# Kernel optimization log

Measured on AMD Instinct MI355X. Metric: run time of the kernel, lower is better.

## Reference

```python
import jax, jax.numpy as jnp
import numpy as np

B, L, D_IN, D_H, D_OUT = 8, 1024, 1024, 1024, 1024


def setup_inputs() -> dict:
    key = jax.random.key(0)
    ks = jax.random.split(key, 9)
    s = 0.02  # weight scale to keep ReLU chain stable
    return {
        "leaves": jax.random.normal(ks[0], (B, L, D_IN), dtype=jnp.float32),
        "V_w": jax.random.normal(ks[1], (D_H, D_IN), dtype=jnp.float32) * s,
        "V_b": jax.random.normal(ks[2], (D_H,), dtype=jnp.float32) * s,
        "U_w": jax.random.normal(ks[3], (D_H, D_H), dtype=jnp.float32) * s,
        "U_b": jax.random.normal(ks[4], (D_H,), dtype=jnp.float32) * s,
        "W_w": jax.random.normal(ks[5], (D_H, D_H), dtype=jnp.float32) * s,
        "W_b": jax.random.normal(ks[6], (D_H,), dtype=jnp.float32) * s,
        "O_w": jax.random.normal(ks[7], (D_OUT, D_H), dtype=jnp.float32) * s,
        "O_b": jax.random.normal(ks[8], (D_OUT,), dtype=jnp.float32) * s,
    }


def reference(leaves, V_w, V_b, U_w, U_b, W_w, W_b, O_w, O_b):
    # Leaf encoding: h_leaf = relu(V(x))            [B, L, H]
    h = jax.nn.relu(jnp.einsum("bli,hi->blh", leaves, V_w) + V_b)
    # Depth-batched recursion over the complete binary tree:
    # combined = relu(U(left) + W(right)); log2(L) levels, node count halves.
    while h.shape[1] > 1:
        left, right = h[:, 0::2], h[:, 1::2]  # [B, n/2, H] each
        h = jax.nn.relu(
            jnp.einsum("bnh,gh->bng", left, U_w) + U_b
            + jnp.einsum("bnh,gh->bng", right, W_w) + W_b
        )
    root = h[:, 0]  # [B, H]
    logits = jnp.einsum("bh,oh->bo", root, O_w) + O_b
    return jax.nn.log_softmax(logits, axis=-1)
```

## Files before the change

kernel.cpp:

```cpp
#include <hip/hip_runtime.h>
#include <hip/hip_bf16.h>
#include <math.h>

typedef __bf16 bf16_t;
typedef __bf16 bf16x8 __attribute__((ext_vector_type(8)));
typedef __bf16 bf16x4 __attribute__((ext_vector_type(4)));
typedef float  f32x4  __attribute__((ext_vector_type(4)));

#define GLD_LDS16(g, l)                                                          \
  __builtin_amdgcn_global_load_lds((const __attribute__((address_space(1))) void*)(g), \
                                   (__attribute__((address_space(3))) void*)(l), 16, 0, 0)

__global__ __launch_bounds__(256) void k_cvt_all(const float* __restrict__ leaves,
                                                 const float* __restrict__ V_w,
                                                 const float* __restrict__ O_w,
                                                 const float* __restrict__ U_w,
                                                 const float* __restrict__ W_w,
                                                 const float* __restrict__ U_b,
                                                 const float* __restrict__ W_b,
                                                 bf16_t* __restrict__ leaves_bf,
                                                 bf16_t* __restrict__ Vw_bf,
                                                 bf16_t* __restrict__ Ow_bf,
                                                 bf16_t* __restrict__ UW_bf,
                                                 float* __restrict__ buw) {
  const int gtid = blockIdx.x * 256 + threadIdx.x;
  const int G = gridDim.x * 256;
  for (int i = gtid; i < 2097152; i += G) {
    float4 v = reinterpret_cast<const float4*>(leaves)[i];
    bf16x4 o; o[0] = (bf16_t)v.x; o[1] = (bf16_t)v.y; o[2] = (bf16_t)v.z; o[3] = (bf16_t)v.w;
    reinterpret_cast<bf16x4*>(leaves_bf)[i] = o;
  }
  for (int i = gtid; i < 262144; i += G) {
    float4 v = reinterpret_cast<const float4*>(V_w)[i];
    bf16x4 o; o[0] = (bf16_t)v.x; o[1] = (bf16_t)v.y; o[2] = (bf16_t)v.z; o[3] = (bf16_t)v.w;
    reinterpret_cast<bf16x4*>(Vw_bf)[i] = o;
  }
  for (int i = gtid; i < 262144; i += G) {
    float4 v = reinterpret_cast<const float4*>(O_w)[i];
    bf16x4 o; o[0] = (bf16_t)v.x; o[1] = (bf16_t)v.y; o[2] = (bf16_t)v.z; o[3] = (bf16_t)v.w;
    reinterpret_cast<bf16x4*>(Ow_bf)[i] = o;
  }
  for (int idx = gtid; idx < 524288; idx += G) {
    int i = idx * 4;
    int g = i >> 11;
    int k = i & 2047;
    const float* src = (k < 1024) ? (U_w + g * 1024 + k) : (W_w + g * 1024 + (k - 1024));
    float4 v = *reinterpret_cast<const float4*>(src);
    bf16x4 o; o[0] = (bf16_t)v.x; o[1] = (bf16_t)v.y; o[2] = (bf16_t)v.z; o[3] = (bf16_t)v.w;
    reinterpret_cast<bf16x4*>(UW_bf)[idx] = o;
  }
  if (gtid < 1024) buw[gtid] = U_b[gtid] + W_b[gtid];
}

template <bool SPLIT>
__global__ __launch_bounds__(512, 4) void k_gemm2(
    const bf16_t* __restrict__ A, const bf16_t* __restrict__ Bw,
    const float* __restrict__ bias, bf16_t* __restrict__ C,
    bf16_t* __restrict__ P, int M, int Kstride, int kchunk) {
  constexpr int NB = 5;
  constexpr int VM = 2;
  __shared__ bf16_t As[NB][128 * 32];
  __shared__ bf16_t Bs[NB][128 * 32];

  const int tid = threadIdx.x;
  const int lane = tid & 63;
  const int wave = tid >> 6;
  const int wr = wave >> 2;
  const int wc = wave & 3;
  const int bm = blockIdx.x, bn = blockIdx.y, bz = blockIdx.z;

  const bf16_t* Abase = A + (size_t)bm * 128 * Kstride + (size_t)bz * kchunk;
  const bf16_t* Bbase = Bw + (size_t)bn * 128 * Kstride + (size_t)bz * kchunk;

  f32x4 acc[4][2] = {};
  const int rl = lane & 15, kq = lane >> 4;

  auto stage = [&](int buf, int ko) {
    {
      int c = tid;
      int r = c >> 2, kbp = c & 3;
      int kb = kbp ^ ((r >> 1) & 3);
      GLD_LDS16(Abase + (size_t)r * Kstride + ko + kb * 8, &As[buf][c * 8]);
    }
    {
      int c = tid;
      int r = c >> 2, kbp = c & 3;
      int kb = kbp ^ ((r >> 1) & 3);
      GLD_LDS16(Bbase + (size_t)r * Kstride + ko + kb * 8, &Bs[buf][c * 8]);
    }
  };

  const int kiters = kchunk >> 5;
  stage(0, 0);
  if (kiters > 1) stage(1, 32);
  if (kiters > 2) stage(2, 64);
  if (kiters > 3) stage(3, 96);

  int cur = 0;
  for (int t = 0; t < kiters; ++t) {
    const int nin = kiters - 1 - t;
    if (nin >= 3)      asm volatile("s_waitcnt vmcnt(%0)" :: "i"(3 * VM) : "memory");
    else if (nin == 2) asm volatile("s_waitcnt vmcnt(%0)" :: "i"(2 * VM) : "memory");
    else if (nin == 1) asm volatile("s_waitcnt vmcnt(%0)" :: "i"(VM) : "memory");
    else               asm volatile("s_waitcnt vmcnt(0)" ::: "memory");
    __builtin_amdgcn_s_barrier();
    __builtin_amdgcn_sched_barrier(0);
    if (t + NB - 1 < kiters) {
      int bnx = cur + NB - 1; if (bnx >= NB) bnx -= NB;
      stage(bnx, (t + NB - 1) * 32);
    }
    bf16x8 af[4], bfr[2];
#pragma unroll
    for (int i = 0; i < 4; ++i) {
      int r = wr * 64 + i * 16 + rl;
      int kbp = kq ^ ((r >> 1) & 3);
      af[i] = *reinterpret_cast<const bf16x8*>(&As[cur][r * 32 + kbp * 8]);
    }
#pragma unroll
    for (int j = 0; j < 2; ++j) {
      int r = wc * 32 + j * 16 + rl;
      int kbp = kq ^ ((r >> 1) & 3);
      bfr[j] = *reinterpret_cast<const bf16x8*>(&Bs[cur][r * 32 + kbp * 8]);
    }
#pragma unroll
    for (int i = 0; i < 4; ++i)
#pragma unroll
      for (int j = 0; j < 2; ++j)
        acc[i][j] = __builtin_amdgcn_mfma_f32_16x16x32_bf16(af[i], bfr[j], acc[i][j], 0, 0, 0);
    if (++cur >= NB) cur = 0;
  }

  const int rq = lane >> 4, cl = lane & 15;
  if (SPLIT) {
    bf16_t* Pp = P + (size_t)bz * M * 1024;
#pragma unroll
    for (int j = 0; j < 2; ++j) {
      int gcol = bn * 128 + wc * 32 + j * 16 + cl;
#pragma unroll
      for (int i = 0; i < 4; ++i) {
        int grow = bm * 128 + wr * 64 + i * 16 + rq * 4;
#pragma unroll
        for (int reg = 0; reg < 4; ++reg)
          Pp[(size_t)(grow + reg) * 1024 + gcol] = (bf16_t)acc[i][j][reg];
      }
    }
  } else {
#pragma unroll
    for (int j = 0; j < 2; ++j) {
      int gcol = bn * 128 + wc * 32 + j * 16 + cl;
      float bv = bias[gcol];
#pragma unroll
      for (int i = 0; i < 4; ++i) {
        int grow = bm * 128 + wr * 64 + i * 16 + rq * 4;
#pragma unroll
        for (int reg = 0; reg < 4; ++reg) {
          float v = acc[i][j][reg] + bv;
          v = v > 0.0f ? v : 0.0f;
          C[(size_t)(grow + reg) * 1024 + gcol] = (bf16_t)v;
        }
      }
    }
  }
}

template <int TM, int TN, bool SPLIT>
__global__ __launch_bounds__(256, 3) void k_gemm(
    const bf16_t* __restrict__ A, const bf16_t* __restrict__ Bw,
    const float* __restrict__ bias, bf16_t* __restrict__ C,
    bf16_t* __restrict__ P, int M, int Kstride, int kchunk) {
  constexpr int MI = TM / 32;
  constexpr int NJ = TN / 32;
  constexpr int VM = TM / 64 + TN / 64;
  constexpr int NB = 4;
  __shared__ bf16_t As[NB][TM * 32];
  __shared__ bf16_t Bs[NB][TN * 32];

  const int tid = threadIdx.x;
  const int lane = tid & 63;
  const int wave = tid >> 6;
  const int wr = wave >> 1, wc = wave & 1;
  const int bm = blockIdx.x, bn = blockIdx.y, bz = blockIdx.z;

  const bf16_t* Abase = A + (size_t)bm * TM * Kstride + (size_t)bz * kchunk;
  const bf16_t* Bbase = Bw + (size_t)bn * TN * Kstride + (size_t)bz * kchunk;

  f32x4 acc[MI][NJ] = {};
  const int rl = lane & 15, kq = lane >> 4;

  auto stage = [&](int buf, int ko) {
#pragma unroll
    for (int it = 0; it < TM / 64; ++it) {
      int c = tid + 256 * it;
      int r = c >> 2, kbp = c & 3;
      int kb = kbp ^ ((r >> 1) & 3);
      GLD_LDS16(Abase + (size_t)r * Kstride + ko + kb * 8, &As[buf][c * 8]);
    }
#pragma unroll
    for (int it = 0; it < TN / 64; ++it) {
      int c = tid + 256 * it;
      int r = c >> 2, kbp = c & 3;
      int kb = kbp ^ ((r >> 1) & 3);
      GLD_LDS16(Bbase + (size_t)r * Kstride + ko + kb * 8, &Bs[buf][c * 8]);
    }
  };

  const int kiters = kchunk >> 5;
  stage(0, 0);
  if (kiters > 1) stage(1, 32);
  if (kiters > 2) stage(2, 64);

  int cur = 0;
  for (int t = 0; t < kiters; ++t) {
    const int nin = kiters - 1 - t;
    if (nin >= 2)      asm volatile("s_waitcnt vmcnt(%0)" :: "i"(2 * VM) : "memory");
    else if (nin == 1) asm volatile("s_waitcnt vmcnt(%0)" :: "i"(VM) : "memory");
    else               asm volatile("s_waitcnt vmcnt(0)" ::: "memory");
    __builtin_amdgcn_s_barrier();
    __builtin_amdgcn_sched_barrier(0);
    if (t + NB - 1 < kiters) {
      int bnx = cur + NB - 1; if (bnx >= NB) bnx -= NB;
      stage(bnx, (t + NB - 1) * 32);
    }
    bf16x8 af[MI], bfr[NJ];
#pragma unroll
    for (int i = 0; i < MI; ++i) {
      int r = wr * (TM / 2) + i * 16 + rl;
      int kbp = kq ^ ((r >> 1) & 3);
      af[i] = *reinterpret_cast<const bf16x8*>(&As[cur][r * 32 + kbp * 8]);
    }
#pragma unroll
    for (int j = 0; j < NJ; ++j) {
      int r = wc * (TN / 2) + j * 16 + rl;
      int kbp = kq ^ ((r >> 1) & 3);
      bfr[j] = *reinterpret_cast<const bf16x8*>(&Bs[cur][r * 32 + kbp * 8]);
    }
#pragma unroll
    for (int i = 0; i < MI; ++i)
#pragma unroll
      for (int j = 0; j < NJ; ++j)
        acc[i][j] = __builtin_amdgcn_mfma_f32_16x16x32_bf16(af[i], bfr[j], acc[i][j], 0, 0, 0);
    if (++cur >= NB) cur = 0;
  }

  const int rq = lane >> 4, cl = lane & 15;
  if (SPLIT) {
    bf16_t* Pp = P + (size_t)bz * M * 1024;
#pragma unroll
    for (int j = 0; j < NJ; ++j) {
      int gcol = bn * TN + wc * (TN / 2) + j * 16 + cl;
#pragma unroll
      for (int i = 0; i < MI; ++i) {
        int grow = bm * TM + wr * (TM / 2) + i * 16 + rq * 4;
#pragma unroll
        for (int reg = 0; reg < 4; ++reg)
          if (grow + reg < M)
            Pp[(size_t)(grow + reg) * 1024 + gcol] = (bf16_t)acc[i][j][reg];
      }
    }
  } else {
#pragma unroll
    for (int j = 0; j < NJ; ++j) {
      int gcol = bn * TN + wc * (TN / 2) + j * 16 + cl;
      float bv = bias[gcol];
#pragma unroll
      for (int i = 0; i < MI; ++i) {
        int grow = bm * TM + wr * (TM / 2) + i * 16 + rq * 4;
#pragma unroll
        for (int reg = 0; reg < 4; ++reg) {
          float v = acc[i][j][reg] + bv;
          v = v > 0.0f ? v : 0.0f;
          C[(size_t)(grow + reg) * 1024 + gcol] = (bf16_t)v;
        }
      }
    }
  }
}

__global__ __launch_bounds__(256) void k_reduce(const bf16_t* __restrict__ P,
                                                const float* __restrict__ bias,
                                                bf16_t* __restrict__ C, int M, int ks) {
  constexpr int N = 1024;
  int idx = blockIdx.x * 256 + threadIdx.x;
  int col = (idx * 4) & (N - 1);
  int row = (idx * 4) >> 10;
  float s0 = 0.0f, s1 = 0.0f, s2 = 0.0f, s3 = 0.0f;
  for (int z = 0; z < ks; ++z) {
    bf16x4 v = *reinterpret_cast<const bf16x4*>(P + ((size_t)z * M + row) * N + col);
    s0 += (float)v[0]; s1 += (float)v[1]; s2 += (float)v[2]; s3 += (float)v[3];
  }
  float4 b = *reinterpret_cast<const float4*>(bias + col);
  bf16x4 o;
  o[0] = (bf16_t)fmaxf(s0 + b.x, 0.0f);
  o[1] = (bf16_t)fmaxf(s1 + b.y, 0.0f);
  o[2] = (bf16_t)fmaxf(s2 + b.z, 0.0f);
  o[3] = (bf16_t)fmaxf(s3 + b.w, 0.0f);
  reinterpret_cast<bf16x4*>(C)[idx] = o;
}

template <int KK, bool RELU, bool F32OUT>
__global__ __launch_bounds__(256) void k_tail(const bf16_t* __restrict__ A,
                                              const bf16_t* __restrict__ Bw,
                                              const float* __restrict__ bias,
                                              void* __restrict__ Cout, int M) {
  constexpr int N = 1024;
  constexpr int KPL = KK / 64;
  const int lane = threadIdx.x & 63;
  const int gw = blockIdx.x * 4 + (threadIdx.x >> 6);
  const int n = gw & (N - 1);
  const int mbase = (gw >> 10) * 8;
  const int k0 = lane * KPL;

  float bv[KPL];
  const bf16_t* bp = Bw + (size_t)n * KK + k0;
#pragma unroll
  for (int q = 0; q < KPL / 8; ++q) {
    bf16x8 v = *reinterpret_cast<const bf16x8*>(bp + q * 8);
#pragma unroll
    for (int j = 0; j < 8; ++j) bv[q * 8 + j] = (float)v[j];
  }

  float acc[8];
#pragma unroll
  for (int m = 0; m < 8; ++m) {
    const bf16_t* ap = A + (size_t)(mbase + m) * KK + k0;
    float s = 0.0f;
#pragma unroll
    for (int q = 0; q < KPL / 8; ++q) {
      bf16x8 v = *reinterpret_cast<const bf16x8*>(ap + q * 8);
#pragma unroll
      for (int j = 0; j < 8; ++j) s += (float)v[j] * bv[q * 8 + j];
    }
    acc[m] = s;
  }
#pragma unroll
  for (int m = 0; m < 8; ++m) {
#pragma unroll
    for (int off = 32; off >= 1; off >>= 1) acc[m] += __shfl_xor(acc[m], off, 64);
  }
  if (lane < 8 && mbase + lane < M) {
    float v = acc[lane] + bias[n];
    if (RELU) v = v > 0.0f ? v : 0.0f;
    if (F32OUT) ((float*)Cout)[(size_t)(mbase + lane) * N + n] = v;
    else        ((bf16_t*)Cout)[(size_t)(mbase + lane) * N + n] = (bf16_t)v;
  }
}

__global__ __launch_bounds__(256) void k_logsoftmax(const float* __restrict__ logits,
                                                    float* __restrict__ out) {
  int b = blockIdx.x;
  const float* x = logits + b * 1024;
  int tid = threadIdx.x;
  int wave = tid >> 6, lane = tid & 63;
  __shared__ float red[8];

  float m = -1e30f;
  for (int i = tid; i < 1024; i += 256) m = fmaxf(m, x[i]);
#pragma unroll
  for (int off = 32; off >= 1; off >>= 1) m = fmaxf(m, __shfl_xor(m, off, 64));
  if (lane == 0) red[wave] = m;
  __syncthreads();
  m = fmaxf(fmaxf(red[0], red[1]), fmaxf(red[2], red[3]));
  float s = 0.0f;
  for (int i = tid; i < 1024; i += 256) s += expf(x[i] - m);
#pragma unroll
  for (int off = 32; off >= 1; off >>= 1) s += __shfl_xor(s, off, 64);
  if (lane == 0) red[wave] = s;
  __syncthreads();
  float lse = m + logf(red[0] + red[1] + red[2] + red[3]);
  for (int i = tid; i < 1024; i += 256) out[b * 1024 + i] = x[i] - lse;
}

extern "C" void kernel_launch(void* const* d_in, const int* in_sizes, int n_in,
                              void* d_out, int out_size, void* d_ws, size_t ws_size,
                              hipStream_t stream) {
  const float* leaves = (const float*)d_in[0];
  const float* V_w = (const float*)d_in[1];
  const float* V_b = (const float*)d_in[2];
  const float* U_w = (const float*)d_in[3];
  const float* U_b = (const float*)d_in[4];
  const float* W_w = (const float*)d_in[5];
  const float* W_b = (const float*)d_in[6];
  const float* O_w = (const float*)d_in[7];
  const float* O_b = (const float*)d_in[8];
  float* out = (float*)d_out;

  char* ws = (char*)d_ws;
  size_t off = 0;
  auto alloc = [&](size_t bytes) -> void* {
    off = (off + 255) & ~(size_t)255;
    void* p = ws + off;
    off += bytes;
    return p;
  };

  const size_t MB16 = (size_t)8192 * 1024 * 2;
  bf16_t* leaves_bf = (bf16_t*)alloc(MB16);
  bf16_t* Vw_bf = (bf16_t*)alloc((size_t)1024 * 1024 * 2);
  bf16_t* UW_bf = (bf16_t*)alloc((size_t)2 * 1024 * 1024 * 2);
  bf16_t* Ow_bf = (bf16_t*)alloc((size_t)1024 * 1024 * 2);
  float* buw = (float*)alloc(1024 * 4);
  bf16_t* hA = (bf16_t*)alloc(MB16);
  float* logits = (float*)alloc(8 * 1024 * 4);
  bf16_t* Pbuf = (bf16_t*)alloc((size_t)8 * 4096 * 1024 * 2);
  (void)ws_size; (void)in_sizes; (void)n_in; (void)out_size;

  k_cvt_all<<<2048, 256, 0, stream>>>(leaves, V_w, O_w, U_w, W_w, U_b, W_b,
                                      leaves_bf, Vw_bf, Ow_bf, UW_bf, buw);

  k_gemm2<false><<<dim3(64, 8), 512, 0, stream>>>(
      leaves_bf, Vw_bf, V_b, hA, nullptr, 8192, 1024, 1024);

  bf16_t* src = hA;
  bf16_t* dst = leaves_bf;
  auto swap = [&]() { bf16_t* t = src; src = dst; dst = t; };

  k_gemm2<true><<<dim3(32, 8, 2), 512, 0, stream>>>(
      src, UW_bf, nullptr, nullptr, Pbuf, 4096, 2048, 1024);
  k_reduce<<<4096 * 1024 / 4 / 256, 256, 0, stream>>>(Pbuf, buw, dst, 4096, 2);
  swap();
  k_gemm<64, 128, false><<<dim3(32, 8), 256, 0, stream>>>(
      src, UW_bf, buw, dst, nullptr, 2048, 2048, 2048);
  swap();
  k_gemm<64, 128, true><<<dim3(16, 8, 4), 256, 0, stream>>>(
      src, UW_bf, nullptr, nullptr, Pbuf, 1024, 2048, 512);
  k_reduce<<<1024 * 1024 / 4 / 256, 256, 0, stream>>>(Pbuf, buw, dst, 1024, 4);
  swap();
  k_gemm<64, 128, true><<<dim3(8, 8, 4), 256, 0, stream>>>(
      src, UW_bf, nullptr, nullptr, Pbuf, 512, 2048, 512);
  k_reduce<<<512 * 1024 / 4 / 256, 256, 0, stream>>>(Pbuf, buw, dst, 512, 4);
  swap();
  k_gemm<64, 128, true><<<dim3(4, 8, 8), 256, 0, stream>>>(
      src, UW_bf, nullptr, nullptr, Pbuf, 256, 2048, 256);
  k_reduce<<<256 * 1024 / 4 / 256, 256, 0, stream>>>(Pbuf, buw, dst, 256, 8);
  swap();
  k_gemm<64, 128, true><<<dim3(2, 8, 8), 256, 0, stream>>>(
      src, UW_bf, nullptr, nullptr, Pbuf, 128, 2048, 256);
  k_reduce<<<128 * 1024 / 4 / 256, 256, 0, stream>>>(Pbuf, buw, dst, 128, 8);
  swap();
  k_gemm<64, 128, true><<<dim3(1, 8, 16), 256, 0, stream>>>(
      src, UW_bf, nullptr, nullptr, Pbuf, 64, 2048, 128);
  k_reduce<<<64 * 1024 / 4 / 256, 256, 0, stream>>>(Pbuf, buw, dst, 64, 16);
  swap();
  k_gemm<64, 128, true><<<dim3(1, 8, 16), 256, 0, stream>>>(
      src, UW_bf, nullptr, nullptr, Pbuf, 32, 2048, 128);
  k_reduce<<<32 * 1024 / 4 / 256, 256, 0, stream>>>(Pbuf, buw, dst, 32, 16);
  swap();
  for (int M = 16; M >= 8; M >>= 1) {
    int blocks = (M / 8) * 1024 / 4;
    k_tail<2048, true, false><<<blocks, 256, 0, stream>>>(src, UW_bf, buw, dst, M);
    swap();
  }

  k_tail<1024, false, true><<<256, 256, 0, stream>>>(src, Ow_bf, O_b, logits, 8);
  k_logsoftmax<<<8, 256, 0, stream>>>(logits, out);
}
```

Baseline: 203.0 us.

## Rework GEMM wave tiling to 4 waves, add BK=64 small-tile kernel, split level two

The 128x128 GEMM now uses 4 waves, each computing a 64x64 sub-tile, instead of 8 waves each computing 64x32. That doubles per-wave register reuse of the A fragments. The 64x128 kernel now stages K=64 per stage with a wider XOR swizzle and 3 buffers, which halves the number of barrier iterations. The 2048-row level now uses a 2-way split-K plus a reduce pass instead of a single full-K kernel, to put more blocks in flight. Fewer waves per block lowers latency hiding, and the extra reduce pass adds memory traffic.

```diff
diff --git a/kernel.cpp b/kernel.cpp
--- a/kernel.cpp
+++ b/kernel.cpp
@@ -53,42 +53,45 @@
 }
 
 template <bool SPLIT>
-__global__ __launch_bounds__(512, 4) void k_gemm2(
+__global__ __launch_bounds__(256, 2) void k_gemm(
     const bf16_t* __restrict__ A, const bf16_t* __restrict__ Bw,
     const float* __restrict__ bias, bf16_t* __restrict__ C,
     bf16_t* __restrict__ P, int M, int Kstride, int kchunk) {
+  constexpr int VM = 3;
   constexpr int NB = 5;
-  constexpr int VM = 2;
   __shared__ bf16_t As[NB][128 * 32];
   __shared__ bf16_t Bs[NB][128 * 32];
 
   const int tid = threadIdx.x;
   const int lane = tid & 63;
   const int wave = tid >> 6;
-  const int wr = wave >> 2;
-  const int wc = wave & 3;
+  const int wr = wave >> 1, wc = wave & 1;
   const int bm = blockIdx.x, bn = blockIdx.y, bz = blockIdx.z;
 
   const bf16_t* Abase = A + (size_t)bm * 128 * Kstride + (size_t)bz * kchunk;
   const bf16_t* Bbase = Bw + (size_t)bn * 128 * Kstride + (size_t)bz * kchunk;
 
-  f32x4 acc[4][2] = {};
+  f32x4 acc[4][4] = {};
   const int rl = lane & 15, kq = lane >> 4;
+  constexpr int VMS = 4;
 
   auto stage = [&](int buf, int ko) {
-    {
-      int c = tid;
+#pragma unroll
+    for (int it = 0; it < 2; ++it) {
+      int c = tid + 256 * it;
       int r = c >> 2, kbp = c & 3;
       int kb = kbp ^ ((r >> 1) & 3);
       GLD_LDS16(Abase + (size_t)r * Kstride + ko + kb * 8, &As[buf][c * 8]);
     }
-    {
-      int c = tid;
+#pragma unroll
+    for (int it = 0; it < 2; ++it) {
+      int c = tid + 256 * it;
       int r = c >> 2, kbp = c & 3;
       int kb = kbp ^ ((r >> 1) & 3);
       GLD_LDS16(Bbase + (size_t)r * Kstride + ko + kb * 8, &Bs[buf][c * 8]);
     }
   };
+  (void)VM;
 
   const int kiters = kchunk >> 5;
   stage(0, 0);
@@ -99,9 +102,9 @@
   int cur = 0;
   for (int t = 0; t < kiters; ++t) {
     const int nin = kiters - 1 - t;
-    if (nin >= 3)      asm volatile("s_waitcnt vmcnt(%0)" :: "i"(3 * VM) : "memory");
-    else if (nin == 2) asm volatile("s_waitcnt vmcnt(%0)" :: "i"(2 * VM) : "memory");
-    else if (nin == 1) asm volatile("s_waitcnt vmcnt(%0)" :: "i"(VM) : "memory");
+    if (nin >= 3)      asm volatile("s_waitcnt vmcnt(%0)" :: "i"(3 * VMS) : "memory");
+    else if (nin == 2) asm volatile("s_waitcnt vmcnt(%0)" :: "i"(2 * VMS) : "memory");
+    else if (nin == 1) asm volatile("s_waitcnt vmcnt(%0)" :: "i"(VMS) : "memory");
     else               asm volatile("s_waitcnt vmcnt(0)" ::: "memory");
     __builtin_amdgcn_s_barrier();
     __builtin_amdgcn_sched_barrier(0);
@@ -109,7 +112,7 @@
       int bnx = cur + NB - 1; if (bnx >= NB) bnx -= NB;
       stage(bnx, (t + NB - 1) * 32);
     }
-    bf16x8 af[4], bfr[2];
+    bf16x8 af[4], bfr[4];
 #pragma unroll
     for (int i = 0; i < 4; ++i) {
       int r = wr * 64 + i * 16 + rl;
@@ -117,15 +120,15 @@
       af[i] = *reinterpret_cast<const bf16x8*>(&As[cur][r * 32 + kbp * 8]);
     }
 #pragma unroll
-    for (int j = 0; j < 2; ++j) {
-      int r = wc * 32 + j * 16 + rl;
+    for (int j = 0; j < 4; ++j) {
+      int r = wc * 64 + j * 16 + rl;
       int kbp = kq ^ ((r >> 1) & 3);
       bfr[j] = *reinterpret_cast<const bf16x8*>(&Bs[cur][r * 32 + kbp * 8]);
     }
 #pragma unroll
     for (int i = 0; i < 4; ++i)
 #pragma unroll
-      for (int j = 0; j < 2; ++j)
+      for (int j = 0; j < 4; ++j)
         acc[i][j] = __builtin_amdgcn_mfma_f32_16x16x32_bf16(af[i], bfr[j], acc[i][j], 0, 0, 0);
     if (++cur >= NB) cur = 0;
   }
@@ -134,8 +137,8 @@
   if (SPLIT) {
     bf16_t* Pp = P + (size_t)bz * M * 1024;
 #pragma unroll
-    for (int j = 0; j < 2; ++j) {
-      int gcol = bn * 128 + wc * 32 + j * 16 + cl;
+    for (int j = 0; j < 4; ++j) {
+      int gcol = bn * 128 + wc * 64 + j * 16 + cl;
 #pragma unroll
       for (int i = 0; i < 4; ++i) {
         int grow = bm * 128 + wr * 64 + i * 16 + rq * 4;
@@ -146,8 +149,8 @@
     }
   } else {
 #pragma unroll
-    for (int j = 0; j < 2; ++j) {
-      int gcol = bn * 128 + wc * 32 + j * 16 + cl;
+    for (int j = 0; j < 4; ++j) {
+      int gcol = bn * 128 + wc * 64 + j * 16 + cl;
       float bv = bias[gcol];
 #pragma unroll
       for (int i = 0; i < 4; ++i) {
@@ -163,17 +166,15 @@
   }
 }
 
-template <int TM, int TN, bool SPLIT>
-__global__ __launch_bounds__(256, 3) void k_gemm(
+template <bool SPLIT>
+__global__ __launch_bounds__(256, 2) void k_gemm64(
     const bf16_t* __restrict__ A, const bf16_t* __restrict__ Bw,
     const float* __restrict__ bias, bf16_t* __restrict__ C,
     bf16_t* __restrict__ P, int M, int Kstride, int kchunk) {
-  constexpr int MI = TM / 32;
-  constexpr int NJ = TN / 32;
-  constexpr int VM = TM / 64 + TN / 64;
-  constexpr int NB = 4;
-  __shared__ bf16_t As[NB][TM * 32];
-  __shared__ bf16_t Bs[NB][TN * 32];
+  constexpr int VM = 6;
+  constexpr int NB = 3;
+  __shared__ bf16_t As[NB][64 * 64];
+  __shared__ bf16_t Bs[NB][128 * 64];
 
   const int tid = threadIdx.x;
   const int lane = tid & 63;
@@ -181,76 +182,77 @@
   const int wr = wave >> 1, wc = wave & 1;
   const int bm = blockIdx.x, bn = blockIdx.y, bz = blockIdx.z;
 
-  const bf16_t* Abase = A + (size_t)bm * TM * Kstride + (size_t)bz * kchunk;
-  const bf16_t* Bbase = Bw + (size_t)bn * TN * Kstride + (size_t)bz * kchunk;
-
-  f32x4 acc[MI][NJ] = {};
+  const bf16_t* Abase = A + (size_t)bm * 64 * Kstride + (size_t)bz * kchunk;
+  const bf16_t* Bbase = Bw + (size_t)bn * 128 * Kstride + (size_t)bz * kchunk;
+
+  f32x4 acc[2][4] = {};
   const int rl = lane & 15, kq = lane >> 4;
 
   auto stage = [&](int buf, int ko) {
 #pragma unroll
-    for (int it = 0; it < TM / 64; ++it) {
+    for (int it = 0; it < 2; ++it) {
       int c = tid + 256 * it;
-      int r = c >> 2, kbp = c & 3;
-      int kb = kbp ^ ((r >> 1) & 3);
+      int r = c >> 3, ch = c & 7;
+      int kb = ch ^ ((r >> 1) & 7);
       GLD_LDS16(Abase + (size_t)r * Kstride + ko + kb * 8, &As[buf][c * 8]);
     }
 #pragma unroll
-    for (int it = 0; it < TN / 64; ++it) {
+    for (int it = 0; it < 4; ++it) {
       int c = tid + 256 * it;
-      int r = c >> 2, kbp = c & 3;
-      int kb = kbp ^ ((r >> 1) & 3);
+      int r = c >> 3, ch = c & 7;
+      int kb = ch ^ ((r >> 1) & 7);
       GLD_LDS16(Bbase + (size_t)r * Kstride + ko + kb * 8, &Bs[buf][c * 8]);
     }
   };
 
-  const int kiters = kchunk >> 5;
+  const int kiters = kchunk >> 6;
   stage(0, 0);
-  if (kiters > 1) stage(1, 32);
-  if (kiters > 2) stage(2, 64);
+  if (kiters > 1) stage(1, 64);
 
   int cur = 0;
   for (int t = 0; t < kiters; ++t) {
     const int nin = kiters - 1 - t;
-    if (nin >= 2)      asm volatile("s_waitcnt vmcnt(%0)" :: "i"(2 * VM) : "memory");
-    else if (nin == 1) asm volatile("s_waitcnt vmcnt(%0)" :: "i"(VM) : "memory");
-    else               asm volatile("s_waitcnt vmcnt(0)" ::: "memory");
+    if (nin >= 1) asm volatile("s_waitcnt vmcnt(%0)" :: "i"(VM) : "memory");
+    else          asm volatile("s_waitcnt vmcnt(0)" ::: "memory");
     __builtin_amdgcn_s_barrier();
     __builtin_amdgcn_sched_barrier(0);
-    if (t + NB - 1 < kiters) {
-      int bnx = cur + NB - 1; if (bnx >= NB) bnx -= NB;
-      stage(bnx, (t + NB - 1) * 32);
-    }
-    bf16x8 af[MI], bfr[NJ];
-#pragma unroll
-    for (int i = 0; i < MI; ++i) {
-      int r = wr * (TM / 2) + i * 16 + rl;
-      int kbp = kq ^ ((r >> 1) & 3);
-      af[i] = *reinterpret_cast<const bf16x8*>(&As[cur][r * 32 + kbp * 8]);
-    }
-#pragma unroll
-    for (int j = 0; j < NJ; ++j) {
-      int r = wc * (TN / 2) + j * 16 + rl;
-      int kbp = kq ^ ((r >> 1) & 3);
-      bfr[j] = *reinterpret_cast<const bf16x8*>(&Bs[cur][r * 32 + kbp * 8]);
-    }
-#pragma unroll
-    for (int i = 0; i < MI; ++i)
-#pragma unroll
-      for (int j = 0; j < NJ; ++j)
-        acc[i][j] = __builtin_amdgcn_mfma_f32_16x16x32_bf16(af[i], bfr[j], acc[i][j], 0, 0, 0);
-    if (++cur >= NB) cur = 0;
+    if (t + 2 < kiters) {
+      int b2 = cur + 2; if (b2 >= 3) b2 -= 3;
+      stage(b2, (t + 2) * 64);
+    }
+#pragma unroll
+    for (int kk = 0; kk < 2; ++kk) {
+      bf16x8 af[2], bfr[4];
+#pragma unroll
+      for (int i = 0; i < 2; ++i) {
+        int r = wr * 32 + i * 16 + rl;
+        int ch = ((kk << 2) | kq) ^ ((r >> 1) & 7);
+        af[i] = *reinterpret_cast<const bf16x8*>(&As[cur][r * 64 + ch * 8]);
+      }
+#pragma unroll
+      for (int j = 0; j < 4; ++j) {
+        int r = wc * 64 + j * 16 + rl;
+        int ch = ((kk << 2) | kq) ^ ((r >> 1) & 7);
+        bfr[j] = *reinterpret_cast<const bf16x8*>(&Bs[cur][r * 64 + ch * 8]);
+      }
+#pragma unroll
+      for (int i = 0; i < 2; ++i)
+#pragma unroll
+        for (int j = 0; j < 4; ++j)
+          acc[i][j] = __builtin_amdgcn_mfma_f32_16x16x32_bf16(af[i], bfr[j], acc[i][j], 0, 0, 0);
+    }
+    if (++cur >= 3) cur = 0;
   }
 
   const int rq = lane >> 4, cl = lane & 15;
   if (SPLIT) {
     bf16_t* Pp = P + (size_t)bz * M * 1024;
 #pragma unroll
-    for (int j = 0; j < NJ; ++j) {
-      int gcol = bn * TN + wc * (TN / 2) + j * 16 + cl;
-#pragma unroll
-      for (int i = 0; i < MI; ++i) {
-        int grow = bm * TM + wr * (TM / 2) + i * 16 + rq * 4;
+    for (int j = 0; j < 4; ++j) {
+      int gcol = bn * 128 + wc * 64 + j * 16 + cl;
+#pragma unroll
+      for (int i = 0; i < 2; ++i) {
+        int grow = bm * 64 + wr * 32 + i * 16 + rq * 4;
 #pragma unroll
         for (int reg = 0; reg < 4; ++reg)
           if (grow + reg < M)
@@ -259,12 +261,12 @@
     }
   } else {
 #pragma unroll
-    for (int j = 0; j < NJ; ++j) {
-      int gcol = bn * TN + wc * (TN / 2) + j * 16 + cl;
+    for (int j = 0; j < 4; ++j) {
+      int gcol = bn * 128 + wc * 64 + j * 16 + cl;
       float bv = bias[gcol];
 #pragma unroll
-      for (int i = 0; i < MI; ++i) {
-        int grow = bm * TM + wr * (TM / 2) + i * 16 + rq * 4;
+      for (int i = 0; i < 2; ++i) {
+        int grow = bm * 64 + wr * 32 + i * 16 + rq * 4;
 #pragma unroll
         for (int reg = 0; reg < 4; ++reg) {
           float v = acc[i][j][reg] + bv;
@@ -407,41 +409,42 @@
   k_cvt_all<<<2048, 256, 0, stream>>>(leaves, V_w, O_w, U_w, W_w, U_b, W_b,
                                       leaves_bf, Vw_bf, Ow_bf, UW_bf, buw);
 
-  k_gemm2<false><<<dim3(64, 8), 512, 0, stream>>>(
+  k_gemm<false><<<dim3(64, 8), 256, 0, stream>>>(
       leaves_bf, Vw_bf, V_b, hA, nullptr, 8192, 1024, 1024);
 
   bf16_t* src = hA;
   bf16_t* dst = leaves_bf;
   auto swap = [&]() { bf16_t* t = src; src = dst; dst = t; };
 
-  k_gemm2<true><<<dim3(32, 8, 2), 512, 0, stream>>>(
+  k_gemm<true><<<dim3(32, 8, 2), 256, 0, stream>>>(
       src, UW_bf, nullptr, nullptr, Pbuf, 4096, 2048, 1024);
   k_reduce<<<4096 * 1024 / 4 / 256, 256, 0, stream>>>(Pbuf, buw, dst, 4096, 2);
   swap();
-  k_gemm<64, 128, false><<<dim3(32, 8), 256, 0, stream>>>(
-      src, UW_bf, buw, dst, nullptr, 2048, 2048, 2048);
-  swap();
-  k_gemm<64, 128, true><<<dim3(16, 8, 4), 256, 0, stream>>>(
+  k_gemm64<true><<<dim3(32, 8, 2), 256, 0, stream>>>(
+      src, UW_bf, nullptr, nullptr, Pbuf, 2048, 2048, 1024);
+  k_reduce<<<2048 * 1024 / 4 / 256, 256, 0, stream>>>(Pbuf, buw, dst, 2048, 2);
+  swap();
+  k_gemm64<true><<<dim3(16, 8, 4), 256, 0, stream>>>(
       src, UW_bf, nullptr, nullptr, Pbuf, 1024, 2048, 512);
   k_reduce<<<1024 * 1024 / 4 / 256, 256, 0, stream>>>(Pbuf, buw, dst, 1024, 4);
   swap();
-  k_gemm<64, 128, true><<<dim3(8, 8, 4), 256, 0, stream>>>(
+  k_gemm64<true><<<dim3(8, 8, 4), 256, 0, stream>>>(
       src, UW_bf, nullptr, nullptr, Pbuf, 512, 2048, 512);
   k_reduce<<<512 * 1024 / 4 / 256, 256, 0, stream>>>(Pbuf, buw, dst, 512, 4);
   swap();
-  k_gemm<64, 128, true><<<dim3(4, 8, 8), 256, 0, stream>>>(
+  k_gemm64<true><<<dim3(4, 8, 8), 256, 0, stream>>>(
       src, UW_bf, nullptr, nullptr, Pbuf, 256, 2048, 256);
   k_reduce<<<256 * 1024 / 4 / 256, 256, 0, stream>>>(Pbuf, buw, dst, 256, 8);
   swap();
-  k_gemm<64, 128, true><<<dim3(2, 8, 8), 256, 0, stream>>>(
+  k_gemm64<true><<<dim3(2, 8, 8), 256, 0, stream>>>(
       src, UW_bf, nullptr, nullptr, Pbuf, 128, 2048, 256);
   k_reduce<<<128 * 1024 / 4 / 256, 256, 0, stream>>>(Pbuf, buw, dst, 128, 8);
   swap();
-  k_gemm<64, 128, true><<<dim3(1, 8, 16), 256, 0, stream>>>(
+  k_gemm64<true><<<dim3(1, 8, 16), 256, 0, stream>>>(
       src, UW_bf, nullptr, nullptr, Pbuf, 64, 2048, 128);
   k_reduce<<<64 * 1024 / 4 / 256, 256, 0, stream>>>(Pbuf, buw, dst, 64, 16);
   swap();
-  k_gemm<64, 128, true><<<dim3(1, 8, 16), 256, 0, stream>>>(
+  k_gemm64<true><<<dim3(1, 8, 16), 256, 0, stream>>>(
       src, UW_bf, nullptr, nullptr, Pbuf, 32, 2048, 128);
   k_reduce<<<32 * 1024 / 4 / 256, 256, 0, stream>>>(Pbuf, buw, dst, 32, 16);
   swap();
```

After: 188.4 us. 1.08x faster.
